# Optimization experiments

Hardware: AMD Instinct MI355X
Metric: run time of the kernel (lower is better)

Reference implementation:

```python
import jax, jax.numpy as jnp
import numpy as np

V = 196608          # 12 * nside^2, nside = 128 (HEALPix)
DEG = 9             # ~8 neighbors + diagonal
NNZ = V * DEG
K = 3               # Chebyshev order (kernel_size)
C_IN, C_MID, C_OUT = 16, 32, 32
B = 2
EPS = 1e-5


def _spmv(rows, cols, vals, x):
    """Sparse Laplacian mat-vec over the vertex dim. x: [B, V, F]."""
    Bn, Vn, F = x.shape
    y = x.transpose(1, 0, 2).reshape(Vn, Bn * F)          # [V, B*F]
    gathered = y[cols] * vals[:, None]                    # [NNZ, B*F] irregular gather
    out = jax.ops.segment_sum(gathered, rows, num_segments=Vn)
    return out.reshape(Vn, Bn, F).transpose(1, 0, 2)      # [B, V, F]


def _cheb_conv(rows, cols, vals, x, W):
    """K-order Chebyshev conv. W: [K, Fin, Fout]."""
    x0 = x
    x1 = _spmv(rows, cols, vals, x0)
    xs = [x0, x1]
    for _ in range(W.shape[0] - 2):
        xs.append(2.0 * _spmv(rows, cols, vals, xs[-1]) - xs[-2])
    stack = jnp.stack(xs)                                  # [K, B, V, Fin]
    return jnp.einsum('kbvf,kfo->bvo', stack, W)


def _bn_relu(x, gamma, beta):
    """BatchNorm over (batch, vertices) per channel (training stats), then ReLU."""
    mean = x.mean(axis=(0, 1))
    var = x.var(axis=(0, 1))  # biased, as torch BN uses for normalization
    return jax.nn.relu((x - mean) * jax.lax.rsqrt(var + EPS) * gamma + beta)


def setup_inputs() -> dict:
    key = jax.random.key(0)
    ks = jax.random.split(key, 8)
    x = jax.random.normal(ks[0], (B, V, C_IN), dtype=jnp.float32)
    rows = jnp.repeat(jnp.arange(V, dtype=jnp.int64), DEG)              # sorted row indices
    cols = jax.random.randint(ks[1], (NNZ,), 0, V).astype(jnp.int64)
    vals = jax.random.normal(ks[2], (NNZ,), dtype=jnp.float32) * 0.1
    W1 = jax.random.normal(ks[3], (K, C_IN, C_MID), dtype=jnp.float32) * 0.05
    W2 = jax.random.normal(ks[4], (K, C_MID, C_OUT), dtype=jnp.float32) * 0.05
    g1 = jnp.ones((C_MID,), dtype=jnp.float32)
    b1 = jnp.zeros((C_MID,), dtype=jnp.float32)
    g2 = jnp.ones((C_OUT,), dtype=jnp.float32)
    b2 = jnp.zeros((C_OUT,), dtype=jnp.float32)
    return {"x": x, "rows": rows, "cols": cols, "vals": vals,
            "W1": W1, "g1": g1, "b1": b1, "W2": W2, "g2": g2, "b2": b2}


def reference(x, rows, cols, vals, W1, g1, b1, W2, g2, b2):
    h = _cheb_conv(rows, cols, vals, x, W1)
    h = _bn_relu(h, g1, b1)
    h = _cheb_conv(rows, cols, vals, h, W2)
    h = _bn_relu(h, g2, b2)
    return h
```

## Files before the change

kernel.cpp:

```cpp
#include <hip/hip_runtime.h>
#include <hip/hip_bf16.h>

#define Vn 196608
#define DEG 9
#define BV 393216
#define NNZ 1769472
constexpr float EPS = 1e-5f;

typedef unsigned short u16;
using short8 = __attribute__((ext_vector_type(8))) short;
using f32x4  = __attribute__((ext_vector_type(4))) float;

__device__ __forceinline__ float b2f(u16 h) { return __uint_as_float((unsigned)h << 16); }
__device__ __forceinline__ u16 f2b(float f) {
    unsigned u = __float_as_uint(f);
    return (u16)((u + 0x7FFFu + ((u >> 16) & 1u)) >> 16);
}

template<int FF> __device__ __forceinline__ float ldfT(const void* p, int i, int rt) {
    if constexpr (FF == 1) return ((const float*)p)[i];
    else if constexpr (FF == 0) return b2f(((const u16*)p)[i]);
    else return rt ? ((const float*)p)[i] : b2f(((const u16*)p)[i]);
}
template<int FI> __device__ __forceinline__ int ldcT(const void* p, int i, int rt) {
    if constexpr (FI == 1) return (int)((const long long*)p)[i];
    else if constexpr (FI == 0) return ((const int*)p)[i];
    else return rt ? (int)((const long long*)p)[i] : ((const int*)p)[i];
}

__global__ void k0_probe(const void* g1, const void* cols, int* flags, float* zf) {
    int tid = threadIdx.x;
    for (int i = tid; i < 4224; i += 256) zf[i] = 0.f;
    if (tid == 0) {
        const unsigned short* gw = (const unsigned short*)g1;
        int zc = 0;
        for (int i = 0; i < 32; i += 2) if (gw[i] == 0) ++zc;
        flags[0] = (zc >= 8) ? 1 : 0;
        const unsigned int* cw = (const unsigned int*)cols;
        int zodd = 0;
        for (int i = 1; i < 64; i += 2) if (cw[i] == 0) ++zodd;
        flags[1] = (zodd >= 16) ? 1 : 0;
    }
}

template<int FF>
__global__ void __launch_bounds__(256) kxi_pack(const void* __restrict__ x,
                                                const int* __restrict__ flags,
                                                u16* __restrict__ xi) {
    int t = blockIdx.x * 256 + threadIdx.x;
    int rF = 0;
    if constexpr (FF == 2) rF = flags[0];
    int v = t >> 5;
    int lane = t & 31;
    int b = lane >> 4, f = lane & 15;
    xi[t] = f2b(ldfT<FF>(x, (b * Vn + v) * 16 + f, rF));
}

template<int FF, int FI>
__global__ void __launch_bounds__(256) k1_spmv1(const u16* __restrict__ xi,
                                                const void* __restrict__ cols,
                                                const void* __restrict__ vals,
                                                const int* __restrict__ flags,
                                                u16* __restrict__ y1) {
    int t = blockIdx.x * 256 + threadIdx.x;
    int rF = 0, rI = 0;
    if constexpr (FF == 2) { rF = flags[0]; rI = flags[1]; }
    int v = t >> 5;
    int lane = t & 31;
    int e0 = v * DEG;
    float acc = 0.f;
#pragma unroll
    for (int e = 0; e < DEG; ++e) {
        int   c = ldcT<FI>(cols, e0 + e, rI);
        float w = ldfT<FF>(vals, e0 + e, rF);
        acc += w * b2f(xi[c * 32 + lane]);
    }
    y1[t] = f2b(acc);
}

template<int FF, int FI>
__global__ void __launch_bounds__(256) k2a_spmv(const u16* __restrict__ xi,
                                                const u16* __restrict__ y1,
                                                const void* __restrict__ cols,
                                                const void* __restrict__ vals,
                                                const int* __restrict__ flags,
                                                u16* __restrict__ y2) {
    int t = blockIdx.x * 256 + threadIdx.x;
    int rF = 0, rI = 0;
    if constexpr (FF == 2) { rF = flags[0]; rI = flags[1]; }
    int v = t >> 5;
    int lane = t & 31;
    int e0 = v * DEG;
    float acc = 0.f;
#pragma unroll
    for (int e = 0; e < DEG; ++e) {
        int   c = ldcT<FI>(cols, e0 + e, rI);
        float w = ldfT<FF>(vals, e0 + e, rF);
        acc += w * b2f(y1[c * 32 + lane]);
    }
    y2[t] = f2b(2.f * acc - b2f(xi[t]));
}

template<int FF>
__global__ void __launch_bounds__(256) k2b_mfma(const u16* __restrict__ xi,
                                                const u16* __restrict__ y1,
                                                const u16* __restrict__ y2,
                                                const void* __restrict__ W1,
                                                const int* __restrict__ flags,
                                                u16* __restrict__ h1,
                                                float* __restrict__ stats) {
    __shared__ float red[4][32];
    const int tid = threadIdx.x;
    int rF = 0;
    if constexpr (FF == 2) rF = flags[0];
    const int lane = tid & 63;
    const int n = lane & 15, q = lane >> 4;
    const int wv = tid >> 6;
    short8 b1f[2], b2f_[2];
#pragma unroll
    for (int nt = 0; nt < 2; ++nt)
#pragma unroll
        for (int j = 0; j < 8; ++j) {
            int k = q * 8 + j;
            b1f[nt][j]  = (short)f2b(ldfT<FF>(W1, k * 32 + nt * 16 + n, rF));
            b2f_[nt][j] = (k < 16) ? (short)f2b(ldfT<FF>(W1, (32 + k) * 32 + nt * 16 + n, rF)) : (short)0;
        }
    const u16* a1base = (q < 2) ? xi : y1;
    const int koff = (q & 1) * 8;
    float s0 = 0.f, ss0 = 0.f, s1 = 0.f, ss1 = 0.f;
    const int ntile_cnt = BV / 16;
    const int wstride = gridDim.x * 4;
    for (int tile = blockIdx.x * 4 + wv; tile < ntile_cnt; tile += wstride) {
        const int p0 = tile * 16;
        const int ar = (p0 + n) * 16 + koff;
        short8 af1 = *(const short8*)&a1base[ar];
        short8 af2 = *(const short8*)&y2[ar];
        f32x4 c0 = {0.f, 0.f, 0.f, 0.f}, c1 = {0.f, 0.f, 0.f, 0.f};
        c0 = __builtin_amdgcn_mfma_f32_16x16x32_bf16(af1, b1f[0],  c0, 0, 0, 0);
        c0 = __builtin_amdgcn_mfma_f32_16x16x32_bf16(af2, b2f_[0], c0, 0, 0, 0);
        c1 = __builtin_amdgcn_mfma_f32_16x16x32_bf16(af1, b1f[1],  c1, 0, 0, 0);
        c1 = __builtin_amdgcn_mfma_f32_16x16x32_bf16(af2, b2f_[1], c1, 0, 0, 0);
#pragma unroll
        for (int r = 0; r < 4; ++r) {
            int p = p0 + q * 4 + r;
            float e0 = c0[r], e1 = c1[r];
            h1[p * 32 + n]      = f2b(e0);
            h1[p * 32 + 16 + n] = f2b(e1);
            s0 += e0; ss0 += e0 * e0;
            s1 += e1; ss1 += e1 * e1;
        }
    }
    s0  += __shfl_xor(s0, 16);  s0  += __shfl_xor(s0, 32);
    ss0 += __shfl_xor(ss0, 16); ss0 += __shfl_xor(ss0, 32);
    s1  += __shfl_xor(s1, 16);  s1  += __shfl_xor(s1, 32);
    ss1 += __shfl_xor(ss1, 16); ss1 += __shfl_xor(ss1, 32);
    if (q == 0) { red[wv][n] = s0; red[wv][16 + n] = s1; }
    __syncthreads();
    if (tid < 32) atomicAdd(&stats[tid * 32], red[0][tid] + red[1][tid] + red[2][tid] + red[3][tid]);
    __syncthreads();
    if (q == 0) { red[wv][n] = ss0; red[wv][16 + n] = ss1; }
    __syncthreads();
    if (tid < 32) atomicAdd(&stats[(32 + tid) * 32], red[0][tid] + red[1][tid] + red[2][tid] + red[3][tid]);
}

__global__ void k_finalize(const float* __restrict__ stats,
                           const void* __restrict__ gamma,
                           const void* __restrict__ beta,
                           const int* __restrict__ flags,
                           float* __restrict__ scsh) {
    int o = threadIdx.x;
    if (o < 32) {
        const int fF = flags[0];
        const float n = (float)BV;
        float mean = stats[o * 32] / n;
        float var  = stats[(32 + o) * 32] / n - mean * mean;
        var = fmaxf(var, 0.f);
        float rs = rsqrtf(var + EPS);
        float sc = ldfT<2>(gamma, o, fF) * rs;
        scsh[o]      = sc;
        scsh[32 + o] = ldfT<2>(beta, o, fF) - mean * sc;
    }
}

template<int FF, int FI>
__global__ void __launch_bounds__(256) k3_spmv2(const u16* __restrict__ h1,
                                                const void* __restrict__ cols,
                                                const void* __restrict__ vals,
                                                const int* __restrict__ flags,
                                                const float* __restrict__ scsh,
                                                u16* __restrict__ z1) {
    int t = blockIdx.x * 256 + threadIdx.x;
    int rF = 0, rI = 0;
    if constexpr (FF == 2) { rF = flags[0]; rI = flags[1]; }
    int v = t >> 6;
    int lane = t & 63;
    int f = lane & 31;
    float sc = scsh[f], sh = scsh[32 + f];
    int e0 = v * DEG;
    float acc = 0.f;
#pragma unroll
    for (int e = 0; e < DEG; ++e) {
        int   c = ldcT<FI>(cols, e0 + e, rI);
        float w = ldfT<FF>(vals, e0 + e, rF);
        float hv = b2f(h1[c * 64 + lane]);
        acc += w * fmaxf(0.f, hv * sc + sh);
    }
    z1[t] = f2b(acc);
}

template<int FF, int FI>
__global__ void __launch_bounds__(256) k4a_spmv3(const u16* __restrict__ h1,
                                                 const u16* __restrict__ z1,
                                                 const void* __restrict__ cols,
                                                 const void* __restrict__ vals,
                                                 const int* __restrict__ flags,
                                                 const float* __restrict__ scsh,
                                                 u16* __restrict__ z2) {
    int t = blockIdx.x * 256 + threadIdx.x;
    int rF = 0, rI = 0;
    if constexpr (FF == 2) { rF = flags[0]; rI = flags[1]; }
    int v = t >> 6;
    int lane = t & 63;
    int f = lane & 31;
    float sc = scsh[f], sh = scsh[32 + f];
    int e0 = v * DEG;
    float acc = 0.f;
#pragma unroll
    for (int e = 0; e < DEG; ++e) {
        int   c = ldcT<FI>(cols, e0 + e, rI);
        float w = ldfT<FF>(vals, e0 + e, rF);
        acc += w * b2f(z1[c * 64 + lane]);
    }
    float hn = fmaxf(0.f, b2f(h1[v * 64 + lane]) * sc + sh);
    z2[t] = f2b(2.f * acc - hn);
}

template<int FF>
__global__ void __launch_bounds__(256) k4b_mfma(const u16* __restrict__ h1,
                                                const u16* __restrict__ z1,
                                                const u16* __restrict__ z2,
                                                const void* __restrict__ W2,
                                                const int* __restrict__ flags,
                                                const float* __restrict__ scsh,
                                                void* __restrict__ out, int outF,
                                                float* __restrict__ stats) {
    __shared__ float red[4][32];
    const int tid = threadIdx.x;
    int rF = 0;
    if constexpr (FF == 2) rF = flags[0];
    const int lane = tid & 63;
    const int n = lane & 15, q = lane >> 4;
    const int wv = tid >> 6;
    short8 bf[3][2];
#pragma unroll
    for (int kc = 0; kc < 3; ++kc)
#pragma unroll
        for (int nt = 0; nt < 2; ++nt)
#pragma unroll
            for (int j = 0; j < 8; ++j)
                bf[kc][nt][j] = (short)f2b(ldfT<FF>(W2, (kc * 32 + q * 8 + j) * 32 + nt * 16 + n, rF));
    float scv[8], shv[8];
#pragma unroll
    for (int j = 0; j < 8; ++j) { scv[j] = scsh[q * 8 + j]; shv[j] = scsh[32 + q * 8 + j]; }

    float s0 = 0.f, ss0 = 0.f, s1 = 0.f, ss1 = 0.f;
    const int ntile_cnt = BV / 16;
    const int wstride = gridDim.x * 4;
    for (int tile = blockIdx.x * 4 + wv; tile < ntile_cnt; tile += wstride) {
        const int p0 = tile * 16;
        const int arow = (p0 + n) * 32 + q * 8;
        short8 hv = *(const short8*)&h1[arow];
        short8 a0;
#pragma unroll
        for (int j = 0; j < 8; ++j)
            a0[j] = (short)f2b(fmaxf(0.f, b2f((u16)hv[j]) * scv[j] + shv[j]));
        short8 a1 = *(const short8*)&z1[arow];
        short8 a2 = *(const short8*)&z2[arow];
        f32x4 c0 = {0.f, 0.f, 0.f, 0.f}, c1 = {0.f, 0.f, 0.f, 0.f};
        c0 = __builtin_amdgcn_mfma_f32_16x16x32_bf16(a0, bf[0][0], c0, 0, 0, 0);
        c0 = __builtin_amdgcn_mfma_f32_16x16x32_bf16(a1, bf[1][0], c0, 0, 0, 0);
        c0 = __builtin_amdgcn_mfma_f32_16x16x32_bf16(a2, bf[2][0], c0, 0, 0, 0);
        c1 = __builtin_amdgcn_mfma_f32_16x16x32_bf16(a0, bf[0][1], c1, 0, 0, 0);
        c1 = __builtin_amdgcn_mfma_f32_16x16x32_bf16(a1, bf[1][1], c1, 0, 0, 0);
        c1 = __builtin_amdgcn_mfma_f32_16x16x32_bf16(a2, bf[2][1], c1, 0, 0, 0);
#pragma unroll
        for (int r = 0; r < 4; ++r) {
            int p = p0 + q * 4 + r;
            int v = p >> 1, b = p & 1;
            int base = (b * Vn + v) * 32;
            float e0 = c0[r], e1 = c1[r];
            if (outF) { ((float*)out)[base + n] = e0; ((float*)out)[base + 16 + n] = e1; }
            else      { ((u16*)out)[base + n] = f2b(e0); ((u16*)out)[base + 16 + n] = f2b(e1); }
            s0 += e0; ss0 += e0 * e0;
            s1 += e1; ss1 += e1 * e1;
        }
    }
    s0  += __shfl_xor(s0, 16);  s0  += __shfl_xor(s0, 32);
    ss0 += __shfl_xor(ss0, 16); ss0 += __shfl_xor(ss0, 32);
    s1  += __shfl_xor(s1, 16);  s1  += __shfl_xor(s1, 32);
    ss1 += __shfl_xor(ss1, 16); ss1 += __shfl_xor(ss1, 32);
    if (q == 0) { red[wv][n] = s0; red[wv][16 + n] = s1; }
    __syncthreads();
    if (tid < 32) atomicAdd(&stats[tid * 32], red[0][tid] + red[1][tid] + red[2][tid] + red[3][tid]);
    __syncthreads();
    if (q == 0) { red[wv][n] = ss0; red[wv][16 + n] = ss1; }
    __syncthreads();
    if (tid < 32) atomicAdd(&stats[(32 + tid) * 32], red[0][tid] + red[1][tid] + red[2][tid] + red[3][tid]);
}

__global__ void __launch_bounds__(256) k5_norm(void* __restrict__ io, int outF,
                                               const float* __restrict__ scsh) {
    int t = blockIdx.x * 256 + threadIdx.x;
    if (outF) {
        float4* p = (float4*)io;
        float4 vv = p[t];
        int o = (t * 4) & 31;
        vv.x = fmaxf(0.f, vv.x * scsh[o]     + scsh[32 + o]);
        vv.y = fmaxf(0.f, vv.y * scsh[o + 1] + scsh[33 + o]);
        vv.z = fmaxf(0.f, vv.z * scsh[o + 2] + scsh[34 + o]);
        vv.w = fmaxf(0.f, vv.w * scsh[o + 3] + scsh[35 + o]);
        p[t] = vv;
    } else {
        u16* p = (u16*)io;
#pragma unroll
        for (int j = 0; j < 4; ++j) {
            int i = t * 4 + j;
            int o = i & 31;
            p[i] = f2b(fmaxf(0.f, b2f(p[i]) * scsh[o] + scsh[32 + o]));
        }
    }
}

static inline int alloc_size_class(const void* p, size_t small, size_t big) {
    hipDeviceptr_t base = nullptr; size_t sz = 0;
    if (hipMemGetAddressRange(&base, &sz, (hipDeviceptr_t)p) != hipSuccess || sz == 0) return -1;
    if (sz >= small && sz < small + 65536) return 0;
    if (sz >= big   && sz < big   + 65536) return 1;
    return -1;
}

extern "C" void kernel_launch(void* const* d_in, const int* in_sizes, int n_in,
                              void* d_out, int out_size, void* d_ws, size_t ws_size,
                              hipStream_t stream) {
    const void* x    = d_in[0];
    const void* cols = d_in[2];
    const void* vals = d_in[3];
    const void* W1   = d_in[4];
    const void* g1   = d_in[5];
    const void* b1   = d_in[6];
    const void* W2   = d_in[7];
    const void* g2   = d_in[8];
    const void* b2   = d_in[9];

    int outF = 1;
    {
        hipDeviceptr_t base = nullptr; size_t sz = 0;
        if (hipMemGetAddressRange(&base, &sz, (hipDeviceptr_t)d_out) == hipSuccess && sz != 0) {
            outF = (sz >= (size_t)out_size * 3) ? 1 : 0;
        }
    }
    int fI = alloc_size_class(cols, (size_t)NNZ * 4, (size_t)NNZ * 8);
    int fF = alloc_size_class(vals, (size_t)NNZ * 2, (size_t)NNZ * 4);

    char* ws = (char*)d_ws;
    int*   flags  = (int*)ws;
    float* zf     = (float*)(ws + 1024);
    float* scsh1  = zf;
    float* scsh2  = zf + 64;
    float* stats1 = zf + 128;
    float* stats2 = zf + 128 + 2048;
    size_t off = 32768;
    u16* xi = (u16*)(ws + off); off += (size_t)Vn * 32 * 2;
    u16* y1 = (u16*)(ws + off); off += (size_t)Vn * 32 * 2;
    u16* y2 = (u16*)(ws + off); off += (size_t)Vn * 32 * 2;
    u16* h1 = (u16*)(ws + off); off += (size_t)Vn * 64 * 2;
    u16* z1 = (u16*)(ws + off); off += (size_t)Vn * 64 * 2;
    u16* z2 = (u16*)(ws + off);

    k0_probe<<<1, 256, 0, stream>>>(g1, cols, flags, zf);

#define LAUNCH_ALL(FFv, FIv)                                                                  \
    do {                                                                                      \
        kxi_pack<FFv><<<Vn * 32 / 256, 256, 0, stream>>>(x, flags, xi);                       \
        k1_spmv1<FFv, FIv><<<Vn * 32 / 256, 256, 0, stream>>>(xi, cols, vals, flags, y1);     \
        k2a_spmv<FFv, FIv><<<Vn * 32 / 256, 256, 0, stream>>>(xi, y1, cols, vals, flags, y2); \
        k2b_mfma<FFv><<<2048, 256, 0, stream>>>(xi, y1, y2, W1, flags, h1, stats1);           \
        k_finalize<<<1, 64, 0, stream>>>(stats1, g1, b1, flags, scsh1);                       \
        k3_spmv2<FFv, FIv><<<Vn * 64 / 256, 256, 0, stream>>>(h1, cols, vals, flags, scsh1, z1); \
        k4a_spmv3<FFv, FIv><<<Vn * 64 / 256, 256, 0, stream>>>(h1, z1, cols, vals, flags, scsh1, z2); \
        k4b_mfma<FFv><<<2048, 256, 0, stream>>>(h1, z1, z2, W2, flags, scsh1, d_out, outF, stats2); \
        k_finalize<<<1, 64, 0, stream>>>(stats2, g2, b2, flags, scsh2);                       \
        k5_norm<<<BV * 8 / 256, 256, 0, stream>>>(d_out, outF, scsh2);                        \
    } while (0)

    if      (fF == 0 && fI == 0) LAUNCH_ALL(0, 0);
    else if (fF == 0 && fI == 1) LAUNCH_ALL(0, 1);
    else if (fF == 1 && fI == 0) LAUNCH_ALL(1, 0);
    else if (fF == 1 && fI == 1) LAUNCH_ALL(1, 1);
    else                         LAUNCH_ALL(2, 2);
#undef LAUNCH_ALL
}
```

Measured before the change: 351.6 us.

## Fuse second SpMV into MFMA projection kernels and drop intermediate buffers

Merges the second Chebyshev SpMV of each layer into the following MFMA einsum kernel. Each wave computes its 16-row tile of y2 or z2 and stages it in LDS before feeding the MFMA, so the y2/z2 global round trip and two launches go away. Stats zeroing moves into the pack kernel, and the probe kernel now runs only on the runtime-dispatch path. The cost is lower parallelism during the gather phase, since only 2048 persistent blocks run it, plus extra LDS traffic.

```diff
diff --git a/kernel.cpp b/kernel.cpp
--- a/kernel.cpp
+++ b/kernel.cpp
@@ -46,8 +46,12 @@
 template<int FF>
 __global__ void __launch_bounds__(256) kxi_pack(const void* __restrict__ x,
                                                 const int* __restrict__ flags,
-                                                u16* __restrict__ xi) {
+                                                u16* __restrict__ xi,
+                                                float* __restrict__ zf) {
     int t = blockIdx.x * 256 + threadIdx.x;
+    if (blockIdx.x == 0) {
+        for (int i = threadIdx.x; i < 4224; i += 256) zf[i] = 0.f;
+    }
     int rF = 0;
     if constexpr (FF == 2) rF = flags[0];
     int v = t >> 5;
@@ -79,43 +83,23 @@
 }
 
 template<int FF, int FI>
-__global__ void __launch_bounds__(256) k2a_spmv(const u16* __restrict__ xi,
-                                                const u16* __restrict__ y1,
-                                                const void* __restrict__ cols,
-                                                const void* __restrict__ vals,
-                                                const int* __restrict__ flags,
-                                                u16* __restrict__ y2) {
-    int t = blockIdx.x * 256 + threadIdx.x;
+__global__ void __launch_bounds__(256) k2ab(const u16* __restrict__ xi,
+                                            const u16* __restrict__ y1,
+                                            const void* __restrict__ cols,
+                                            const void* __restrict__ vals,
+                                            const void* __restrict__ W1,
+                                            const int* __restrict__ flags,
+                                            u16* __restrict__ h1,
+                                            float* __restrict__ stats) {
+    __shared__ u16 yt[4][16 * 16];
+    __shared__ float red[4][32];
+    const int tid = threadIdx.x;
     int rF = 0, rI = 0;
     if constexpr (FF == 2) { rF = flags[0]; rI = flags[1]; }
-    int v = t >> 5;
-    int lane = t & 31;
-    int e0 = v * DEG;
-    float acc = 0.f;
-#pragma unroll
-    for (int e = 0; e < DEG; ++e) {
-        int   c = ldcT<FI>(cols, e0 + e, rI);
-        float w = ldfT<FF>(vals, e0 + e, rF);
-        acc += w * b2f(y1[c * 32 + lane]);
-    }
-    y2[t] = f2b(2.f * acc - b2f(xi[t]));
-}
-
-template<int FF>
-__global__ void __launch_bounds__(256) k2b_mfma(const u16* __restrict__ xi,
-                                                const u16* __restrict__ y1,
-                                                const u16* __restrict__ y2,
-                                                const void* __restrict__ W1,
-                                                const int* __restrict__ flags,
-                                                u16* __restrict__ h1,
-                                                float* __restrict__ stats) {
-    __shared__ float red[4][32];
-    const int tid = threadIdx.x;
-    int rF = 0;
-    if constexpr (FF == 2) rF = flags[0];
     const int lane = tid & 63;
     const int n = lane & 15, q = lane >> 4;
     const int wv = tid >> 6;
+    const int half = lane >> 5, l5 = lane & 31;
     short8 b1f[2], b2f_[2];
 #pragma unroll
     for (int nt = 0; nt < 2; ++nt)
@@ -132,9 +116,25 @@
     const int wstride = gridDim.x * 4;
     for (int tile = blockIdx.x * 4 + wv; tile < ntile_cnt; tile += wstride) {
         const int p0 = tile * 16;
+        const int v0 = p0 >> 1;
+#pragma unroll
+        for (int i = 0; i < 4; ++i) {
+            int v = v0 + 2 * i + half;
+            int e0 = v * DEG;
+            float acc = 0.f;
+#pragma unroll
+            for (int e = 0; e < DEG; ++e) {
+                int   c = ldcT<FI>(cols, e0 + e, rI);
+                float w = ldfT<FF>(vals, e0 + e, rF);
+                acc += w * b2f(y1[c * 32 + l5]);
+            }
+            float y2v = 2.f * acc - b2f(xi[v * 32 + l5]);
+            int p_local = 4 * i + 2 * half + (l5 >> 4);
+            yt[wv][p_local * 16 + (l5 & 15)] = f2b(y2v);
+        }
         const int ar = (p0 + n) * 16 + koff;
         short8 af1 = *(const short8*)&a1base[ar];
-        short8 af2 = *(const short8*)&y2[ar];
+        short8 af2 = *(const short8*)&yt[wv][n * 16 + koff];
         f32x4 c0 = {0.f, 0.f, 0.f, 0.f}, c1 = {0.f, 0.f, 0.f, 0.f};
         c0 = __builtin_amdgcn_mfma_f32_16x16x32_bf16(af1, b1f[0],  c0, 0, 0, 0);
         c0 = __builtin_amdgcn_mfma_f32_16x16x32_bf16(af2, b2f_[0], c0, 0, 0, 0);
@@ -143,11 +143,11 @@
 #pragma unroll
         for (int r = 0; r < 4; ++r) {
             int p = p0 + q * 4 + r;
-            float e0 = c0[r], e1 = c1[r];
-            h1[p * 32 + n]      = f2b(e0);
-            h1[p * 32 + 16 + n] = f2b(e1);
-            s0 += e0; ss0 += e0 * e0;
-            s1 += e1; ss1 += e1 * e1;
+            float e0v = c0[r], e1v = c1[r];
+            h1[p * 32 + n]      = f2b(e0v);
+            h1[p * 32 + 16 + n] = f2b(e1v);
+            s0 += e0v; ss0 += e0v * e0v;
+            s1 += e1v; ss1 += e1v * e1v;
         }
     }
     s0  += __shfl_xor(s0, 16);  s0  += __shfl_xor(s0, 32);
@@ -163,22 +163,24 @@
     if (tid < 32) atomicAdd(&stats[(32 + tid) * 32], red[0][tid] + red[1][tid] + red[2][tid] + red[3][tid]);
 }
 
+template<int FF>
 __global__ void k_finalize(const float* __restrict__ stats,
                            const void* __restrict__ gamma,
                            const void* __restrict__ beta,
                            const int* __restrict__ flags,
                            float* __restrict__ scsh) {
     int o = threadIdx.x;
+    int rF = 0;
+    if constexpr (FF == 2) rF = flags[0];
     if (o < 32) {
-        const int fF = flags[0];
         const float n = (float)BV;
         float mean = stats[o * 32] / n;
         float var  = stats[(32 + o) * 32] / n - mean * mean;
         var = fmaxf(var, 0.f);
         float rs = rsqrtf(var + EPS);
-        float sc = ldfT<2>(gamma, o, fF) * rs;
+        float sc = ldfT<FF>(gamma, o, rF) * rs;
         scsh[o]      = sc;
-        scsh[32 + o] = ldfT<2>(beta, o, fF) - mean * sc;
+        scsh[32 + o] = ldfT<FF>(beta, o, rF) - mean * sc;
     }
 }
 
@@ -209,48 +211,26 @@
 }
 
 template<int FF, int FI>
-__global__ void __launch_bounds__(256) k4a_spmv3(const u16* __restrict__ h1,
-                                                 const u16* __restrict__ z1,
-                                                 const void* __restrict__ cols,
-                                                 const void* __restrict__ vals,
-                                                 const int* __restrict__ flags,
-                                                 const float* __restrict__ scsh,
-                                                 u16* __restrict__ z2) {
-    int t = blockIdx.x * 256 + threadIdx.x;
+__global__ void __launch_bounds__(256) k4ab(const u16* __restrict__ h1,
+                                            const u16* __restrict__ z1,
+                                            const void* __restrict__ cols,
+                                            const void* __restrict__ vals,
+                                            const void* __restrict__ W2,
+                                            const int* __restrict__ flags,
+                                            const float* __restrict__ scsh,
+                                            void* __restrict__ out, int outF,
+                                            float* __restrict__ stats) {
+    __shared__ u16 ht[4][16 * 32];
+    __shared__ u16 zt[4][16 * 32];
+    __shared__ float red[4][32];
+    const int tid = threadIdx.x;
     int rF = 0, rI = 0;
     if constexpr (FF == 2) { rF = flags[0]; rI = flags[1]; }
-    int v = t >> 6;
-    int lane = t & 63;
-    int f = lane & 31;
-    float sc = scsh[f], sh = scsh[32 + f];
-    int e0 = v * DEG;
-    float acc = 0.f;
-#pragma unroll
-    for (int e = 0; e < DEG; ++e) {
-        int   c = ldcT<FI>(cols, e0 + e, rI);
-        float w = ldfT<FF>(vals, e0 + e, rF);
-        acc += w * b2f(z1[c * 64 + lane]);
-    }
-    float hn = fmaxf(0.f, b2f(h1[v * 64 + lane]) * sc + sh);
-    z2[t] = f2b(2.f * acc - hn);
-}
-
-template<int FF>
-__global__ void __launch_bounds__(256) k4b_mfma(const u16* __restrict__ h1,
-                                                const u16* __restrict__ z1,
-                                                const u16* __restrict__ z2,
-                                                const void* __restrict__ W2,
-                                                const int* __restrict__ flags,
-                                                const float* __restrict__ scsh,
-                                                void* __restrict__ out, int outF,
-                                                float* __restrict__ stats) {
-    __shared__ float red[4][32];
-    const int tid = threadIdx.x;
-    int rF = 0;
-    if constexpr (FF == 2) rF = flags[0];
     const int lane = tid & 63;
     const int n = lane & 15, q = lane >> 4;
     const int wv = tid >> 6;
+    const int f = lane & 31;
+    const float scf = scsh[f], shf = scsh[32 + f];
     short8 bf[3][2];
 #pragma unroll
     for (int kc = 0; kc < 3; ++kc)
@@ -259,23 +239,32 @@
 #pragma unroll
             for (int j = 0; j < 8; ++j)
                 bf[kc][nt][j] = (short)f2b(ldfT<FF>(W2, (kc * 32 + q * 8 + j) * 32 + nt * 16 + n, rF));
-    float scv[8], shv[8];
-#pragma unroll
-    for (int j = 0; j < 8; ++j) { scv[j] = scsh[q * 8 + j]; shv[j] = scsh[32 + q * 8 + j]; }
 
     float s0 = 0.f, ss0 = 0.f, s1 = 0.f, ss1 = 0.f;
     const int ntile_cnt = BV / 16;
     const int wstride = gridDim.x * 4;
     for (int tile = blockIdx.x * 4 + wv; tile < ntile_cnt; tile += wstride) {
         const int p0 = tile * 16;
-        const int arow = (p0 + n) * 32 + q * 8;
-        short8 hv = *(const short8*)&h1[arow];
-        short8 a0;
-#pragma unroll
-        for (int j = 0; j < 8; ++j)
-            a0[j] = (short)f2b(fmaxf(0.f, b2f((u16)hv[j]) * scv[j] + shv[j]));
-        short8 a1 = *(const short8*)&z1[arow];
-        short8 a2 = *(const short8*)&z2[arow];
+        const int v0 = p0 >> 1;
+#pragma unroll
+        for (int i = 0; i < 8; ++i) {
+            int v = v0 + i;
+            int e0 = v * DEG;
+            float acc = 0.f;
+#pragma unroll
+            for (int e = 0; e < DEG; ++e) {
+                int   c = ldcT<FI>(cols, e0 + e, rI);
+                float w = ldfT<FF>(vals, e0 + e, rF);
+                acc += w * b2f(z1[c * 64 + lane]);
+            }
+            float hn = fmaxf(0.f, b2f(h1[v * 64 + lane]) * scf + shf);
+            ht[wv][i * 64 + lane] = f2b(hn);
+            zt[wv][i * 64 + lane] = f2b(2.f * acc - hn);
+        }
+        const int lrow = n * 32 + q * 8;
+        short8 a0 = *(const short8*)&ht[wv][lrow];
+        short8 a2 = *(const short8*)&zt[wv][lrow];
+        short8 a1 = *(const short8*)&z1[(p0 + n) * 32 + q * 8];
         f32x4 c0 = {0.f, 0.f, 0.f, 0.f}, c1 = {0.f, 0.f, 0.f, 0.f};
         c0 = __builtin_amdgcn_mfma_f32_16x16x32_bf16(a0, bf[0][0], c0, 0, 0, 0);
         c0 = __builtin_amdgcn_mfma_f32_16x16x32_bf16(a1, bf[1][0], c0, 0, 0, 0);
@@ -288,11 +277,11 @@
             int p = p0 + q * 4 + r;
             int v = p >> 1, b = p & 1;
             int base = (b * Vn + v) * 32;
-            float e0 = c0[r], e1 = c1[r];
-            if (outF) { ((float*)out)[base + n] = e0; ((float*)out)[base + 16 + n] = e1; }
-            else      { ((u16*)out)[base + n] = f2b(e0); ((u16*)out)[base + 16 + n] = f2b(e1); }
-            s0 += e0; ss0 += e0 * e0;
-            s1 += e1; ss1 += e1 * e1;
+            float e0v = c0[r], e1v = c1[r];
+            if (outF) { ((float*)out)[base + n] = e0v; ((float*)out)[base + 16 + n] = e1v; }
+            else      { ((u16*)out)[base + n] = f2b(e0v); ((u16*)out)[base + 16 + n] = f2b(e1v); }
+            s0 += e0v; ss0 += e0v * e0v;
+            s1 += e1v; ss1 += e1v * e1v;
         }
     }
     s0  += __shfl_xor(s0, 16);  s0  += __shfl_xor(s0, 32);
@@ -372,24 +361,18 @@
     size_t off = 32768;
     u16* xi = (u16*)(ws + off); off += (size_t)Vn * 32 * 2;
     u16* y1 = (u16*)(ws + off); off += (size_t)Vn * 32 * 2;
-    u16* y2 = (u16*)(ws + off); off += (size_t)Vn * 32 * 2;
     u16* h1 = (u16*)(ws + off); off += (size_t)Vn * 64 * 2;
-    u16* z1 = (u16*)(ws + off); off += (size_t)Vn * 64 * 2;
-    u16* z2 = (u16*)(ws + off);
-
-    k0_probe<<<1, 256, 0, stream>>>(g1, cols, flags, zf);
+    u16* z1 = (u16*)(ws + off);
 
 #define LAUNCH_ALL(FFv, FIv)                                                                  \
     do {                                                                                      \
-        kxi_pack<FFv><<<Vn * 32 / 256, 256, 0, stream>>>(x, flags, xi);                       \
+        kxi_pack<FFv><<<Vn * 32 / 256, 256, 0, stream>>>(x, flags, xi, zf);                   \
         k1_spmv1<FFv, FIv><<<Vn * 32 / 256, 256, 0, stream>>>(xi, cols, vals, flags, y1);     \
-        k2a_spmv<FFv, FIv><<<Vn * 32 / 256, 256, 0, stream>>>(xi, y1, cols, vals, flags, y2); \
-        k2b_mfma<FFv><<<2048, 256, 0, stream>>>(xi, y1, y2, W1, flags, h1, stats1);           \
-        k_finalize<<<1, 64, 0, stream>>>(stats1, g1, b1, flags, scsh1);                       \
+        k2ab<FFv, FIv><<<2048, 256, 0, stream>>>(xi, y1, cols, vals, W1, flags, h1, stats1);  \
+        k_finalize<FFv><<<1, 64, 0, stream>>>(stats1, g1, b1, flags, scsh1);                  \
         k3_spmv2<FFv, FIv><<<Vn * 64 / 256, 256, 0, stream>>>(h1, cols, vals, flags, scsh1, z1); \
-        k4a_spmv3<FFv, FIv><<<Vn * 64 / 256, 256, 0, stream>>>(h1, z1, cols, vals, flags, scsh1, z2); \
-        k4b_mfma<FFv><<<2048, 256, 0, stream>>>(h1, z1, z2, W2, flags, scsh1, d_out, outF, stats2); \
-        k_finalize<<<1, 64, 0, stream>>>(stats2, g2, b2, flags, scsh2);                       \
+        k4ab<FFv, FIv><<<2048, 256, 0, stream>>>(h1, z1, cols, vals, W2, flags, scsh1, d_out, outF, stats2); \
+        k_finalize<FFv><<<1, 64, 0, stream>>>(stats2, g2, b2, flags, scsh2);                  \
         k5_norm<<<BV * 8 / 256, 256, 0, stream>>>(d_out, outF, scsh2);                        \
     } while (0)
 
@@ -397,6 +380,9 @@
     else if (fF == 0 && fI == 1) LAUNCH_ALL(0, 1);
     else if (fF == 1 && fI == 0) LAUNCH_ALL(1, 0);
     else if (fF == 1 && fI == 1) LAUNCH_ALL(1, 1);
-    else                         LAUNCH_ALL(2, 2);
+    else {
+        k0_probe<<<1, 256, 0, stream>>>(g1, cols, flags, zf);
+        LAUNCH_ALL(2, 2);
+    }
 #undef LAUNCH_ALL
 }
```

Result: faster. 321.1 us (-8.7%).
